# Performance work log

Measured on AMD Instinct MI355X. Metric: run time of the kernel, lower is better.

## Reference

```python
import jax, jax.numpy as jnp
import numpy as np


def setup_inputs() -> dict:
    key = jax.random.key(0)
    ks = jax.random.split(key, 9)
    H, A = 1024, 1024
    Ns, Ne, M = 8192, 4096, 8192
    s = 1.0 / np.sqrt(H)
    return {
        "attendee_stmts": jax.random.normal(ks[0], (Ns, H), jnp.float32),
        "attendee_eres": jax.random.normal(ks[1], (Ne, H), jnp.float32),
        "attender": jax.random.normal(ks[2], (M, H), jnp.float32),
        "W_ss": jax.random.normal(ks[3], (H, H), jnp.float32) * s,
        "b_ss": jnp.zeros((H,), jnp.float32),
        "W_es": jax.random.normal(ks[4], (H, H), jnp.float32) * s,
        "b_es": jnp.zeros((H,), jnp.float32),
        "W_lin": jax.random.normal(ks[5], (A, 3 * H), jnp.float32) * (1.0 / np.sqrt(3 * H)),
        "b_lin": jnp.zeros((A,), jnp.float32),
    }


def reference(attendee_stmts, attendee_eres, attender,
              W_ss, b_ss, W_es, b_es, W_lin, b_lin):
    # Bilinear scores: Linear(attendees) @ attender^T -> [N, M]
    scores_ss = (attendee_stmts @ W_ss.T + b_ss) @ attender.T   # [Ns, M]
    scores_es = (attendee_eres @ W_es.T + b_es) @ attender.T    # [Ne, M]
    # Softmax over attendee dim (dim 0), dropout p=0 -> identity
    w_ss = jax.nn.softmax(scores_ss, axis=0)
    w_es = jax.nn.softmax(scores_es, axis=0)
    # Context vectors: weights^T @ attendees -> [M, H]
    ctx_ss = w_ss.T @ attendee_stmts
    ctx_es = w_es.T @ attendee_eres
    # concat + Linear + tanh -> [M, A]
    cat = jnp.concatenate([attender, ctx_ss, ctx_es], axis=-1)  # [M, 3H]
    return jnp.tanh(cat @ W_lin.T + b_lin)
```

## Files before the change

kernel.cpp:

```cpp
#include <hip/hip_runtime.h>
#include <hip/hip_fp16.h>
#include <stdint.h>

typedef _Float16 f16;
typedef _Float16 f16x8 __attribute__((ext_vector_type(8)));
typedef _Float16 f16x4 __attribute__((ext_vector_type(4)));
typedef float f32x4 __attribute__((ext_vector_type(4)));
typedef short s16x8 __attribute__((ext_vector_type(8)));
typedef unsigned short u16x8 __attribute__((ext_vector_type(8)));
typedef unsigned short u16x4 __attribute__((ext_vector_type(4)));

#define DEV __device__ __forceinline__

DEV void gload_lds16(const void* g, void* l) {
    __builtin_amdgcn_global_load_lds(
        (const __attribute__((address_space(1))) void*)g,
        (__attribute__((address_space(3))) void*)l, 16, 0, 0);
}

DEV unsigned short f32_to_bf16(float x) {
    union { float f; unsigned int u; } c; c.f = x;
    unsigned int r = (c.u + 0x7FFFu + ((c.u >> 16) & 1u)) >> 16;
    return (unsigned short)r;
}
DEV float bf16_to_f32(unsigned short h) {
    union { unsigned int u; float f; } c; c.u = ((unsigned int)h) << 16;
    return c.f;
}

DEV void swz_map(int bid, int nx, int ny, int& bm, int& bn) {
    const int xcd = bid & 7;
    const int j = bid >> 3;
    const int py = ny >> 3;
    bm = xcd * py + j / nx;
    bn = j % nx;
}

__global__ __launch_bounds__(256, 2) void gemm_score(
    const float* __restrict__ A, const f16* __restrict__ Bhi,
    const f16* __restrict__ Blo, int ldc, unsigned short* __restrict__ Sp)
{
    __shared__ alignas(16) f16 As_hi[128 * 32];
    __shared__ alignas(16) f16 As_lo[128 * 32];
    __shared__ alignas(16) f16 Bs_hi[128 * 32];
    __shared__ alignas(16) f16 Bs_lo[128 * 32];
    const int t = threadIdx.x;
    const int lane = t & 63;
    const int w = t >> 6;
    const size_t m0 = (size_t)blockIdx.y * 128;
    const size_t n0 = (size_t)blockIdx.x * 128;
    const int wrow = (w >> 1) * 64;
    const int wcol = (w & 1) * 64;

    f32x4 acc[4][4] = {};

    for (int k0 = 0; k0 < 1024; k0 += 32) {
        __syncthreads();
#pragma unroll
        for (int p = 0; p < 4; ++p) {
            const int idx = p * 256 + t;
            const int row = idx >> 3;
            const int col4 = (idx & 7) << 2;
            const f32x4 v = *(const f32x4*)&A[(m0 + row) * 1024 + k0 + col4];
            f16x4 h, l;
#pragma unroll
            for (int j = 0; j < 4; ++j) {
                h[j] = (f16)v[j];
                l[j] = (f16)(v[j] - (float)h[j]);
            }
            *(f16x4*)&As_hi[idx * 4] = h;
            *(f16x4*)&As_lo[idx * 4] = l;
        }
#pragma unroll
        for (int i = 0; i < 2; ++i) {
            const int c = i * 256 + t;
            const int row = c >> 2;
            const int col = (c & 3) << 3;
            const int loff = (i * 256 + w * 64) * 8;
            const size_t gb = (n0 + row) * (size_t)1024 + k0 + col;
            gload_lds16(Bhi + gb, &Bs_hi[loff]);
            gload_lds16(Blo + gb, &Bs_lo[loff]);
        }
        __syncthreads();
        const int fr = lane & 15;
        const int fk = (lane >> 4) << 3;
        f16x8 ah[4], al[4], bh[4], bl[4];
#pragma unroll
        for (int x = 0; x < 4; ++x) {
            ah[x] = *(const f16x8*)&As_hi[(wrow + x * 16 + fr) * 32 + fk];
            al[x] = *(const f16x8*)&As_lo[(wrow + x * 16 + fr) * 32 + fk];
            bh[x] = *(const f16x8*)&Bs_hi[(wcol + x * 16 + fr) * 32 + fk];
            bl[x] = *(const f16x8*)&Bs_lo[(wcol + x * 16 + fr) * 32 + fk];
        }
#pragma unroll
        for (int mi = 0; mi < 4; ++mi)
#pragma unroll
            for (int ni = 0; ni < 4; ++ni) {
                acc[mi][ni] = __builtin_amdgcn_mfma_f32_16x16x32_f16(ah[mi], bh[ni], acc[mi][ni], 0, 0, 0);
                acc[mi][ni] = __builtin_amdgcn_mfma_f32_16x16x32_f16(al[mi], bh[ni], acc[mi][ni], 0, 0, 0);
                acc[mi][ni] = __builtin_amdgcn_mfma_f32_16x16x32_f16(ah[mi], bl[ni], acc[mi][ni], 0, 0, 0);
            }
    }

    const int fr = lane & 15;
    const int fq = lane >> 4;
#pragma unroll
    for (int mi = 0; mi < 4; ++mi)
#pragma unroll
        for (int ni = 0; ni < 4; ++ni)
#pragma unroll
            for (int r = 0; r < 4; ++r) {
                const size_t row = m0 + wrow + mi * 16 + fq * 4 + r;
                const size_t col = n0 + wcol + ni * 16 + fr;
                const float e = __expf(acc[mi][ni][r] - 150.f);
                Sp[row * (size_t)ldc + col] = f32_to_bf16(e);
            }
}

__global__ __launch_bounds__(256, 2) void gemm_proj(
    const float* __restrict__ A, const float* __restrict__ B,
    const float* __restrict__ bias, int ldc,
    f16* __restrict__ Phi, f16* __restrict__ Plo)
{
    __shared__ alignas(16) f16 As_hi[128 * 32];
    __shared__ alignas(16) f16 As_lo[128 * 32];
    __shared__ alignas(16) f16 Bs_hi[128 * 32];
    __shared__ alignas(16) f16 Bs_lo[128 * 32];
    const int t = threadIdx.x;
    const int lane = t & 63;
    const int w = t >> 6;
    const size_t m0 = (size_t)blockIdx.y * 128;
    const size_t n0 = (size_t)blockIdx.x * 128;
    const int wrow = (w >> 1) * 64;
    const int wcol = (w & 1) * 64;

    f32x4 acc[4][4] = {};

    for (int k0 = 0; k0 < 1024; k0 += 32) {
        __syncthreads();
#pragma unroll
        for (int p = 0; p < 4; ++p) {
            const int idx = p * 256 + t;
            const int row = idx >> 3;
            const int col4 = (idx & 7) << 2;
            const f32x4 va = *(const f32x4*)&A[(m0 + row) * 1024 + k0 + col4];
            const f32x4 vb = *(const f32x4*)&B[(n0 + row) * 1024 + k0 + col4];
            f16x4 ha, la, hb, lb;
#pragma unroll
            for (int j = 0; j < 4; ++j) {
                ha[j] = (f16)va[j];
                la[j] = (f16)(va[j] - (float)ha[j]);
                hb[j] = (f16)vb[j];
                lb[j] = (f16)(vb[j] - (float)hb[j]);
            }
            *(f16x4*)&As_hi[idx * 4] = ha;
            *(f16x4*)&As_lo[idx * 4] = la;
            *(f16x4*)&Bs_hi[idx * 4] = hb;
            *(f16x4*)&Bs_lo[idx * 4] = lb;
        }
        __syncthreads();
        const int fr = lane & 15;
        const int fk = (lane >> 4) << 3;
        f16x8 ah[4], al[4], bh[4], bl[4];
#pragma unroll
        for (int x = 0; x < 4; ++x) {
            ah[x] = *(const f16x8*)&As_hi[(wrow + x * 16 + fr) * 32 + fk];
            al[x] = *(const f16x8*)&As_lo[(wrow + x * 16 + fr) * 32 + fk];
            bh[x] = *(const f16x8*)&Bs_hi[(wcol + x * 16 + fr) * 32 + fk];
            bl[x] = *(const f16x8*)&Bs_lo[(wcol + x * 16 + fr) * 32 + fk];
        }
#pragma unroll
        for (int mi = 0; mi < 4; ++mi)
#pragma unroll
            for (int ni = 0; ni < 4; ++ni) {
                acc[mi][ni] = __builtin_amdgcn_mfma_f32_16x16x32_f16(ah[mi], bh[ni], acc[mi][ni], 0, 0, 0);
                acc[mi][ni] = __builtin_amdgcn_mfma_f32_16x16x32_f16(al[mi], bh[ni], acc[mi][ni], 0, 0, 0);
                acc[mi][ni] = __builtin_amdgcn_mfma_f32_16x16x32_f16(ah[mi], bl[ni], acc[mi][ni], 0, 0, 0);
            }
    }

    const int fr = lane & 15;
    const int fq = lane >> 4;
#pragma unroll
    for (int mi = 0; mi < 4; ++mi)
#pragma unroll
        for (int ni = 0; ni < 4; ++ni)
#pragma unroll
            for (int r = 0; r < 4; ++r) {
                const size_t row = m0 + wrow + mi * 16 + fq * 4 + r;
                const size_t col = n0 + wcol + ni * 16 + fr;
                float v = acc[mi][ni][r] + bias[col];
                const f16 h = (f16)v;
                Phi[row * (size_t)ldc + col] = h;
                Plo[row * (size_t)ldc + col] = (f16)(v - (float)h);
            }
}

__global__ __launch_bounds__(256, 4) void gemm_ctx_sk(
    const unsigned short* __restrict__ A, const unsigned short* __restrict__ B,
    const float* __restrict__ isum, int ldk, int K2,
    f16* __restrict__ P0, f16* __restrict__ P1)
{
    __shared__ alignas(16) unsigned short LA[2][128 * 32];
    __shared__ alignas(16) unsigned short LB[2][128 * 32];
    const int t = threadIdx.x;
    const int lane = t & 63;
    const int w = t >> 6;
    const int kh = blockIdx.x >> 9;
    int bm, bn;
    swz_map(blockIdx.x & 511, 8, 64, bm, bn);
    const size_t m0 = (size_t)bm * 128;
    const size_t n0 = (size_t)bn * 128;
    const size_t koff = (size_t)kh * K2;
    const int wrow = (w >> 1) * 64;
    const int wcol = (w & 1) * 64;
    const int fr = lane & 15;
    const int bslot = lane >> 4;
    f16* __restrict__ P = kh ? P1 : P0;

    const int s0 = t, s1 = 256 + t;
    const int r0 = s0 >> 2, c0 = s0 & 3;
    const int r1 = s1 >> 2, c1 = s1 & 3;
    const size_t ga0 = (m0 + r0) * (size_t)ldk + koff + ((c0 ^ (r0 & 3)) << 3);
    const size_t ga1 = (m0 + r1) * (size_t)ldk + koff + ((c1 ^ (r1 & 3)) << 3);
    const size_t gb0 = (n0 + r0) * (size_t)ldk + koff + ((c0 ^ (r0 & 3)) << 3);
    const size_t gb1 = (n0 + r1) * (size_t)ldk + koff + ((c1 ^ (r1 & 3)) << 3);

    f32x4 acc[4][4] = {};

    auto stage = [&](int kt, int b) {
        const int k0 = kt << 5;
        gload_lds16(A + ga0 + k0, &LA[b][(size_t)s0 * 8]);
        gload_lds16(A + ga1 + k0, &LA[b][(size_t)s1 * 8]);
        gload_lds16(B + gb0 + k0, &LB[b][(size_t)s0 * 8]);
        gload_lds16(B + gb1 + k0, &LB[b][(size_t)s1 * 8]);
    };

    auto compute = [&](int b) {
        s16x8 a[4], bb[4];
#pragma unroll
        for (int x = 0; x < 4; ++x) {
            const int ra = wrow + x * 16 + fr;
            const int rb = wcol + x * 16 + fr;
            a[x]  = *(const s16x8*)&LA[b][ra * 32 + ((bslot ^ (ra & 3)) << 3)];
            bb[x] = *(const s16x8*)&LB[b][rb * 32 + ((bslot ^ (rb & 3)) << 3)];
        }
#pragma unroll
        for (int mi = 0; mi < 4; ++mi)
#pragma unroll
            for (int ni = 0; ni < 4; ++ni)
                acc[mi][ni] = __builtin_amdgcn_mfma_f32_16x16x32_bf16(a[mi], bb[ni], acc[mi][ni], 0, 0, 0);
    };

    const int NT = K2 >> 5;
    stage(0, 0);
#pragma unroll 1
    for (int kt = 0; kt < NT; kt += 2) {
        __syncthreads();
        if (kt + 1 < NT) stage(kt + 1, 1);
        __builtin_amdgcn_s_setprio(1);
        compute(0);
        __builtin_amdgcn_s_setprio(0);
        __syncthreads();
        if (kt + 2 < NT) stage(kt + 2, 0);
        __builtin_amdgcn_s_setprio(1);
        compute(1);
        __builtin_amdgcn_s_setprio(0);
    }

    const int fq = lane >> 4;
#pragma unroll
    for (int mi = 0; mi < 4; ++mi)
#pragma unroll
        for (int ni = 0; ni < 4; ++ni)
#pragma unroll
            for (int r = 0; r < 4; ++r) {
                const size_t row = m0 + wrow + mi * 16 + fq * 4 + r;
                const size_t col = n0 + wcol + ni * 16 + fr;
                P[row * 1024 + col] = (f16)(acc[mi][ni][r] * isum[row]);
            }
}

__global__ __launch_bounds__(256, 2) void gemm_final_sk(
    const float* __restrict__ A0, const f16* __restrict__ A1,
    const f16* __restrict__ A2, const f16* __restrict__ B,
    f16* __restrict__ P0, f16* __restrict__ P1)
{
    __shared__ alignas(16) f16 As[128 * 32];
    __shared__ alignas(16) f16 Bs[128 * 32];
    const int t = threadIdx.x;
    const int lane = t & 63;
    const int w = t >> 6;
    const int kh = blockIdx.x >> 9;
    int bm, bn;
    swz_map(blockIdx.x & 511, 8, 64, bm, bn);
    const size_t m0 = (size_t)bm * 128;
    const size_t n0 = (size_t)bn * 128;
    const int wrow = (w >> 1) * 64;
    const int wcol = (w & 1) * 64;
    const int kBeg = kh * 1536;
    f16* __restrict__ P = kh ? P1 : P0;

    f32x4 acc[4][4] = {};

    for (int k0 = kBeg; k0 < kBeg + 1536; k0 += 32) {
        const int kl = k0 & 1023;
        __syncthreads();
        if (k0 < 1024) {
#pragma unroll
            for (int p = 0; p < 4; ++p) {
                const int idx = p * 256 + t;
                const int row = idx >> 3;
                const int col4 = (idx & 7) << 2;
                const f32x4 v = *(const f32x4*)&A0[(m0 + row) * 1024 + kl + col4];
                f16x4 h;
#pragma unroll
                for (int j = 0; j < 4; ++j) h[j] = (f16)v[j];
                *(f16x4*)&As[idx * 4] = h;
            }
        } else {
            const f16* Aseg = (k0 < 2048) ? A1 : A2;
#pragma unroll
            for (int i = 0; i < 2; ++i) {
                const int c = i * 256 + t;
                const int row = c >> 2;
                const int col = (c & 3) << 3;
                const int loff = (i * 256 + w * 64) * 8;
                gload_lds16(Aseg + (m0 + row) * (size_t)1024 + kl + col, &As[loff]);
            }
        }
#pragma unroll
        for (int i = 0; i < 2; ++i) {
            const int c = i * 256 + t;
            const int row = c >> 2;
            const int col = (c & 3) << 3;
            const int loff = (i * 256 + w * 64) * 8;
            gload_lds16(B + (n0 + row) * (size_t)3072 + k0 + col, &Bs[loff]);
        }
        __syncthreads();
        const int fr = lane & 15;
        const int fk = (lane >> 4) << 3;
        f16x8 a[4], b[4];
#pragma unroll
        for (int x = 0; x < 4; ++x) {
            a[x] = *(const f16x8*)&As[(wrow + x * 16 + fr) * 32 + fk];
            b[x] = *(const f16x8*)&Bs[(wcol + x * 16 + fr) * 32 + fk];
        }
#pragma unroll
        for (int mi = 0; mi < 4; ++mi)
#pragma unroll
            for (int ni = 0; ni < 4; ++ni)
                acc[mi][ni] = __builtin_amdgcn_mfma_f32_16x16x32_f16(a[mi], b[ni], acc[mi][ni], 0, 0, 0);
    }

    const int fr = lane & 15;
    const int fq = lane >> 4;
#pragma unroll
    for (int mi = 0; mi < 4; ++mi)
#pragma unroll
        for (int ni = 0; ni < 4; ++ni)
#pragma unroll
            for (int r = 0; r < 4; ++r) {
                const size_t row = m0 + wrow + mi * 16 + fq * 4 + r;
                const size_t col = n0 + wcol + ni * 16 + fr;
                P[row * 1024 + col] = (f16)acc[mi][ni][r];
            }
}

__global__ __launch_bounds__(256) void reduce_add_f16(
    const f16* __restrict__ p0, const f16* __restrict__ p1,
    f16* __restrict__ out, int n8)
{
    for (int i = blockIdx.x * 256 + threadIdx.x; i < n8; i += gridDim.x * 256) {
        const f16x8 a = *(const f16x8*)&p0[(size_t)i * 8];
        const f16x8 b = *(const f16x8*)&p1[(size_t)i * 8];
        f16x8 o;
#pragma unroll
        for (int j = 0; j < 8; ++j) o[j] = (f16)((float)a[j] + (float)b[j]);
        *(f16x8*)&out[(size_t)i * 8] = o;
    }
}

__global__ __launch_bounds__(256) void reduce_tanh_f32(
    const f16* __restrict__ p0, const f16* __restrict__ p1,
    const float* __restrict__ bias, float* __restrict__ out, int n4)
{
    for (int i = blockIdx.x * 256 + threadIdx.x; i < n4; i += gridDim.x * 256) {
        const size_t e = (size_t)i * 4;
        const f16x4 a = *(const f16x4*)&p0[e];
        const f16x4 b = *(const f16x4*)&p1[e];
        f32x4 o;
#pragma unroll
        for (int j = 0; j < 4; ++j)
            o[j] = tanhf((float)a[j] + (float)b[j] + bias[(e + j) & 1023]);
        *(f32x4*)&out[e] = o;
    }
}

template <int C>
__global__ __launch_bounds__(256) void rowsum_inv(
    const unsigned short* __restrict__ E, float* __restrict__ inv)
{
    const unsigned short* e = E + (size_t)blockIdx.x * (C * 2048);
    const int t = threadIdx.x;
    float sm = 0.f;
#pragma unroll
    for (int i = 0; i < C; ++i) {
        const u16x8 v = *(const u16x8*)&e[(t + i * 256) * 8];
#pragma unroll
        for (int j = 0; j < 8; ++j) sm += bf16_to_f32(v[j]);
    }
#pragma unroll
    for (int off = 32; off; off >>= 1) sm += __shfl_xor(sm, off);
    __shared__ float red[4];
    if ((t & 63) == 0) red[t >> 6] = sm;
    __syncthreads();
    if (t == 0) {
        const float s = (red[0] + red[1]) + (red[2] + red[3]);
        inv[blockIdx.x] = 1.f / s;
    }
}

__global__ __launch_bounds__(256) void transpose_f32_to_bf16(
    const float* __restrict__ X, unsigned short* __restrict__ Xt, int N, int H)
{
    __shared__ float tile[64][65];
    const int n0 = blockIdx.x * 64;
    const int h0 = blockIdx.y * 64;
    const int tx = threadIdx.x & 15;
    const int ty = threadIdx.x >> 4;
#pragma unroll
    for (int i = 0; i < 4; ++i) {
        const int r = ty + i * 16;
        const f32x4 vv = *(const f32x4*)&X[(size_t)(n0 + r) * H + h0 + tx * 4];
        tile[r][tx * 4 + 0] = vv[0];
        tile[r][tx * 4 + 1] = vv[1];
        tile[r][tx * 4 + 2] = vv[2];
        tile[r][tx * 4 + 3] = vv[3];
    }
    __syncthreads();
#pragma unroll
    for (int i = 0; i < 4; ++i) {
        const int hh = ty + i * 16;
        u16x4 o;
        o[0] = f32_to_bf16(tile[tx * 4 + 0][hh]);
        o[1] = f32_to_bf16(tile[tx * 4 + 1][hh]);
        o[2] = f32_to_bf16(tile[tx * 4 + 2][hh]);
        o[3] = f32_to_bf16(tile[tx * 4 + 3][hh]);
        *(u16x4*)&Xt[(size_t)(h0 + hh) * N + n0 + tx * 4] = o;
    }
}

__global__ __launch_bounds__(256) void conv_f32_f16(
    const float* __restrict__ X, f16* __restrict__ Y)
{
    const size_t i = ((size_t)blockIdx.x * 256 + threadIdx.x) * 4;
    const f32x4 v = *(const f32x4*)&X[i];
    f16x4 h;
#pragma unroll
    for (int j = 0; j < 4; ++j) h[j] = (f16)v[j];
    *(f16x4*)&Y[i] = h;
}

extern "C" void kernel_launch(void* const* d_in, const int* in_sizes, int n_in,
                              void* d_out, int out_size, void* d_ws, size_t ws_size,
                              hipStream_t stream)
{
    (void)in_sizes; (void)n_in; (void)out_size;
    constexpr int Ns = 8192, Ne = 4096, M = 8192, H = 1024, K3 = 3072, AO = 1024;

    const float* Xss  = (const float*)d_in[0];
    const float* Xes  = (const float*)d_in[1];
    const float* Att  = (const float*)d_in[2];
    const float* Wss  = (const float*)d_in[3];
    const float* bss  = (const float*)d_in[4];
    const float* Wes  = (const float*)d_in[5];
    const float* bes  = (const float*)d_in[6];
    const float* Wlin = (const float*)d_in[7];
    const float* blin = (const float*)d_in[8];
    float* Out = (float*)d_out;

    char* base = (char*)d_ws;
    size_t off = 0;
    auto carve = [&](size_t bytes) {
        char* r = base + off;
        off = (off + bytes + 255) & ~(size_t)255;
        return r;
    };

    f16* Wl16            = (f16*)carve((size_t)AO * K3 * 2);
    unsigned short* Vtss = (unsigned short*)carve((size_t)H * Ns * 2);
    unsigned short* Vtes = (unsigned short*)carve((size_t)H * Ne * 2);
    f16* Pes_hi          = (f16*)carve((size_t)Ne * H * 2);
    f16* Pes_lo          = (f16*)carve((size_t)Ne * H * 2);
    char* PssRg          = carve((size_t)2 * Ns * H * 2);
    char* E              = carve((size_t)M * Ns * 2);
    f16* Ctxss           = (f16*)carve((size_t)M * H * 2);
    f16* Ctxes           = (f16*)carve((size_t)M * H * 2);
    float* isum_ss       = (float*)carve((size_t)M * 4);
    float* isum_es       = (float*)carve((size_t)M * 4);
    if (off > ws_size) return;

    f16* Pss_hi = (f16*)PssRg;
    f16* Pss_lo = Pss_hi + (size_t)Ns * H;
    f16* ctxP0  = (f16*)PssRg;
    f16* ctxP1  = ctxP0 + (size_t)M * H;
    unsigned short* Sss = (unsigned short*)E;
    unsigned short* Ses = (unsigned short*)E;
    f16* fnP0   = (f16*)E;
    f16* fnP1   = fnP0 + (size_t)M * AO;

    const int n8 = (M * H) / 8;
    const int n4 = (M * AO) / 4;

    conv_f32_f16<<<(AO * K3) / 1024, 256, 0, stream>>>(Wlin, Wl16);
    transpose_f32_to_bf16<<<dim3(Ns / 64, H / 64), 256, 0, stream>>>(Xss, Vtss, Ns, H);
    transpose_f32_to_bf16<<<dim3(Ne / 64, H / 64), 256, 0, stream>>>(Xes, Vtes, Ne, H);

    gemm_proj<<<dim3(H / 128, Ns / 128), 256, 0, stream>>>(Xss, Wss, bss, H, Pss_hi, Pss_lo);
    gemm_proj<<<dim3(H / 128, Ne / 128), 256, 0, stream>>>(Xes, Wes, bes, H, Pes_hi, Pes_lo);

    gemm_score<<<dim3(Ns / 128, M / 128), 256, 0, stream>>>(Att, Pss_hi, Pss_lo, Ns, Sss);
    rowsum_inv<4><<<M, 256, 0, stream>>>(Sss, isum_ss);
    gemm_ctx_sk<<<1024, 256, 0, stream>>>(Sss, Vtss, isum_ss, Ns, Ns / 2, ctxP0, ctxP1);
    reduce_add_f16<<<1024, 256, 0, stream>>>(ctxP0, ctxP1, Ctxss, n8);

    gemm_score<<<dim3(Ne / 128, M / 128), 256, 0, stream>>>(Att, Pes_hi, Pes_lo, Ne, Ses);
    rowsum_inv<2><<<M, 256, 0, stream>>>(Ses, isum_es);
    gemm_ctx_sk<<<1024, 256, 0, stream>>>(Ses, Vtes, isum_es, Ne, Ne / 2, ctxP0, ctxP1);
    reduce_add_f16<<<1024, 256, 0, stream>>>(ctxP0, ctxP1, Ctxes, n8);

    gemm_final_sk<<<1024, 256, 0, stream>>>(Att, Ctxss, Ctxes, Wl16, fnP0, fnP1);
    reduce_tanh_f32<<<1024, 256, 0, stream>>>(fnP0, fnP1, blin, Out, n4);
}
```

Baseline: 1.067 ms.

## Fuse softmax row sums into score GEMM epilogue and pre-split attender to f16

```diff
diff --git a/kernel.cpp b/kernel.cpp
--- a/kernel.cpp
+++ b/kernel.cpp
@@ -23,10 +23,6 @@
     unsigned int r = (c.u + 0x7FFFu + ((c.u >> 16) & 1u)) >> 16;
     return (unsigned short)r;
 }
-DEV float bf16_to_f32(unsigned short h) {
-    union { unsigned int u; float f; } c; c.u = ((unsigned int)h) << 16;
-    return c.f;
-}
 
 DEV void swz_map(int bid, int nx, int ny, int& bm, int& bn) {
     const int xcd = bid & 7;
@@ -36,9 +32,36 @@
     bn = j % nx;
 }
 
-__global__ __launch_bounds__(256, 2) void gemm_score(
+DEV void score_epilogue(f32x4 (&acc)[4][4], size_t m0, size_t n0,
+                        int wrow, int wcol, int lane, int ldc,
+                        unsigned short* __restrict__ Sp,
+                        float* __restrict__ rsum)
+{
+    const int fr = lane & 15;
+    const int fq = lane >> 4;
+#pragma unroll
+    for (int mi = 0; mi < 4; ++mi)
+#pragma unroll
+        for (int r = 0; r < 4; ++r) {
+            const size_t row = m0 + wrow + mi * 16 + fq * 4 + r;
+            float rowacc = 0.f;
+#pragma unroll
+            for (int ni = 0; ni < 4; ++ni) {
+                const size_t col = n0 + wcol + ni * 16 + fr;
+                const float e = __expf(acc[mi][ni][r] - 150.f);
+                Sp[row * (size_t)ldc + col] = f32_to_bf16(e);
+                rowacc += e;
+            }
+#pragma unroll
+            for (int m = 1; m < 16; m <<= 1) rowacc += __shfl_xor(rowacc, m);
+            if (fr == 0) atomicAdd(&rsum[row], rowacc);
+        }
+}
+
+__global__ __launch_bounds__(256, 2) void gemm_score_rs(
     const float* __restrict__ A, const f16* __restrict__ Bhi,
-    const f16* __restrict__ Blo, int ldc, unsigned short* __restrict__ Sp)
+    const f16* __restrict__ Blo, int ldc, unsigned short* __restrict__ Sp,
+    float* __restrict__ rsum)
 {
     __shared__ alignas(16) f16 As_hi[128 * 32];
     __shared__ alignas(16) f16 As_lo[128 * 32];
@@ -102,19 +125,65 @@
             }
     }
 
-    const int fr = lane & 15;
-    const int fq = lane >> 4;
-#pragma unroll
-    for (int mi = 0; mi < 4; ++mi)
-#pragma unroll
-        for (int ni = 0; ni < 4; ++ni)
-#pragma unroll
-            for (int r = 0; r < 4; ++r) {
-                const size_t row = m0 + wrow + mi * 16 + fq * 4 + r;
-                const size_t col = n0 + wcol + ni * 16 + fr;
-                const float e = __expf(acc[mi][ni][r] - 150.f);
-                Sp[row * (size_t)ldc + col] = f32_to_bf16(e);
-            }
+    score_epilogue(acc, m0, n0, wrow, wcol, lane, ldc, Sp, rsum);
+}
+
+__global__ __launch_bounds__(256, 2) void gemm_score_4op(
+    const f16* __restrict__ Ahi, const f16* __restrict__ Alo,
+    const f16* __restrict__ Bhi, const f16* __restrict__ Blo,
+    int ldc, unsigned short* __restrict__ Sp, float* __restrict__ rsum)
+{
+    __shared__ alignas(16) f16 As_hi[128 * 32];
+    __shared__ alignas(16) f16 As_lo[128 * 32];
+    __shared__ alignas(16) f16 Bs_hi[128 * 32];
+    __shared__ alignas(16) f16 Bs_lo[128 * 32];
+    const int t = threadIdx.x;
+    const int lane = t & 63;
+    const int w = t >> 6;
+    const size_t m0 = (size_t)blockIdx.y * 128;
+    const size_t n0 = (size_t)blockIdx.x * 128;
+    const int wrow = (w >> 1) * 64;
+    const int wcol = (w & 1) * 64;
+
+    f32x4 acc[4][4] = {};
+
+    for (int k0 = 0; k0 < 1024; k0 += 32) {
+        __syncthreads();
+#pragma unroll
+        for (int i = 0; i < 2; ++i) {
+            const int c = i * 256 + t;
+            const int row = c >> 2;
+            const int col = (c & 3) << 3;
+            const int loff = (i * 256 + w * 64) * 8;
+            const size_t ga = (m0 + row) * (size_t)1024 + k0 + col;
+            const size_t gb = (n0 + row) * (size_t)1024 + k0 + col;
+            gload_lds16(Ahi + ga, &As_hi[loff]);
+            gload_lds16(Alo + ga, &As_lo[loff]);
+            gload_lds16(Bhi + gb, &Bs_hi[loff]);
+            gload_lds16(Blo + gb, &Bs_lo[loff]);
+        }
+        __syncthreads();
+        const int fr = lane & 15;
+        const int fk = (lane >> 4) << 3;
+        f16x8 ah[4], al[4], bh[4], bl[4];
+#pragma unroll
+        for (int x = 0; x < 4; ++x) {
+            ah[x] = *(const f16x8*)&As_hi[(wrow + x * 16 + fr) * 32 + fk];
+            al[x] = *(const f16x8*)&As_lo[(wrow + x * 16 + fr) * 32 + fk];
+            bh[x] = *(const f16x8*)&Bs_hi[(wcol + x * 16 + fr) * 32 + fk];
+            bl[x] = *(const f16x8*)&Bs_lo[(wcol + x * 16 + fr) * 32 + fk];
+        }
+#pragma unroll
+        for (int mi = 0; mi < 4; ++mi)
+#pragma unroll
+            for (int ni = 0; ni < 4; ++ni) {
+                acc[mi][ni] = __builtin_amdgcn_mfma_f32_16x16x32_f16(ah[mi], bh[ni], acc[mi][ni], 0, 0, 0);
+                acc[mi][ni] = __builtin_amdgcn_mfma_f32_16x16x32_f16(al[mi], bh[ni], acc[mi][ni], 0, 0, 0);
+                acc[mi][ni] = __builtin_amdgcn_mfma_f32_16x16x32_f16(ah[mi], bl[ni], acc[mi][ni], 0, 0, 0);
+            }
+    }
+
+    score_epilogue(acc, m0, n0, wrow, wcol, lane, ldc, Sp, rsum);
 }
 
 __global__ __launch_bounds__(256, 2) void gemm_proj(
@@ -397,28 +466,29 @@
     }
 }
 
-template <int C>
-__global__ __launch_bounds__(256) void rowsum_inv(
-    const unsigned short* __restrict__ E, float* __restrict__ inv)
-{
-    const unsigned short* e = E + (size_t)blockIdx.x * (C * 2048);
-    const int t = threadIdx.x;
-    float sm = 0.f;
-#pragma unroll
-    for (int i = 0; i < C; ++i) {
-        const u16x8 v = *(const u16x8*)&e[(t + i * 256) * 8];
-#pragma unroll
-        for (int j = 0; j < 8; ++j) sm += bf16_to_f32(v[j]);
-    }
-#pragma unroll
-    for (int off = 32; off; off >>= 1) sm += __shfl_xor(sm, off);
-    __shared__ float red[4];
-    if ((t & 63) == 0) red[t >> 6] = sm;
-    __syncthreads();
-    if (t == 0) {
-        const float s = (red[0] + red[1]) + (red[2] + red[3]);
-        inv[blockIdx.x] = 1.f / s;
-    }
+__global__ __launch_bounds__(256) void zero_f32(float* __restrict__ p, int n) {
+    const int i = blockIdx.x * 256 + threadIdx.x;
+    if (i < n) p[i] = 0.f;
+}
+
+__global__ __launch_bounds__(256) void inv_f32(float* __restrict__ p, int n) {
+    const int i = blockIdx.x * 256 + threadIdx.x;
+    if (i < n) p[i] = 1.f / p[i];
+}
+
+__global__ __launch_bounds__(256) void split_f32_f16(
+    const float* __restrict__ X, f16* __restrict__ hi, f16* __restrict__ lo)
+{
+    const size_t i = ((size_t)blockIdx.x * 256 + threadIdx.x) * 4;
+    const f32x4 v = *(const f32x4*)&X[i];
+    f16x4 h, l;
+#pragma unroll
+    for (int j = 0; j < 4; ++j) {
+        h[j] = (f16)v[j];
+        l[j] = (f16)(v[j] - (float)h[j]);
+    }
+    *(f16x4*)&hi[i] = h;
+    *(f16x4*)&lo[i] = l;
 }
 
 __global__ __launch_bounds__(256) void transpose_f32_to_bf16(
@@ -491,24 +561,30 @@
     f16* Wl16            = (f16*)carve((size_t)AO * K3 * 2);
     unsigned short* Vtss = (unsigned short*)carve((size_t)H * Ns * 2);
     unsigned short* Vtes = (unsigned short*)carve((size_t)H * Ne * 2);
-    f16* Pes_hi          = (f16*)carve((size_t)Ne * H * 2);
-    f16* Pes_lo          = (f16*)carve((size_t)Ne * H * 2);
+    char* PesRg          = carve((size_t)2 * Ne * H * 2);
     char* PssRg          = carve((size_t)2 * Ns * H * 2);
     char* E              = carve((size_t)M * Ns * 2);
-    f16* Ctxss           = (f16*)carve((size_t)M * H * 2);
+    char* CtxssRg        = carve((size_t)M * H * 2);
     f16* Ctxes           = (f16*)carve((size_t)M * H * 2);
-    float* isum_ss       = (float*)carve((size_t)M * 4);
-    float* isum_es       = (float*)carve((size_t)M * 4);
+    float* sum_ss        = (float*)carve((size_t)M * 4);
+    float* sum_es        = (float*)carve((size_t)M * 4);
     if (off > ws_size) return;
 
+    f16* Pes_hi = (f16*)PesRg;
+    f16* Pes_lo = Pes_hi + (size_t)Ne * H;
+    f16* Att_hi = (f16*)PesRg;
+    f16* Att_lo = (f16*)CtxssRg;
     f16* Pss_hi = (f16*)PssRg;
     f16* Pss_lo = Pss_hi + (size_t)Ns * H;
-    f16* ctxP0  = (f16*)PssRg;
-    f16* ctxP1  = ctxP0 + (size_t)M * H;
+    unsigned short* Ses = (unsigned short*)E;
     unsigned short* Sss = (unsigned short*)E;
-    unsigned short* Ses = (unsigned short*)E;
-    f16* fnP0   = (f16*)E;
-    f16* fnP1   = fnP0 + (size_t)M * AO;
+    f16* esP0  = (f16*)(E + (size_t)M * Ne * 2);
+    f16* esP1  = esP0 + (size_t)M * H;
+    f16* ssP0  = (f16*)PssRg;
+    f16* ssP1  = ssP0 + (size_t)M * H;
+    f16* Ctxss = (f16*)CtxssRg;
+    f16* fnP0  = (f16*)E;
+    f16* fnP1  = fnP0 + (size_t)M * AO;
 
     const int n8 = (M * H) / 8;
     const int n4 = (M * AO) / 4;
@@ -516,19 +592,24 @@
     conv_f32_f16<<<(AO * K3) / 1024, 256, 0, stream>>>(Wlin, Wl16);
     transpose_f32_to_bf16<<<dim3(Ns / 64, H / 64), 256, 0, stream>>>(Xss, Vtss, Ns, H);
     transpose_f32_to_bf16<<<dim3(Ne / 64, H / 64), 256, 0, stream>>>(Xes, Vtes, Ne, H);
+    zero_f32<<<(2 * M) / 256, 256, 0, stream>>>(sum_ss, 2 * M);
 
     gemm_proj<<<dim3(H / 128, Ns / 128), 256, 0, stream>>>(Xss, Wss, bss, H, Pss_hi, Pss_lo);
     gemm_proj<<<dim3(H / 128, Ne / 128), 256, 0, stream>>>(Xes, Wes, bes, H, Pes_hi, Pes_lo);
 
-    gemm_score<<<dim3(Ns / 128, M / 128), 256, 0, stream>>>(Att, Pss_hi, Pss_lo, Ns, Sss);
-    rowsum_inv<4><<<M, 256, 0, stream>>>(Sss, isum_ss);
-    gemm_ctx_sk<<<1024, 256, 0, stream>>>(Sss, Vtss, isum_ss, Ns, Ns / 2, ctxP0, ctxP1);
-    reduce_add_f16<<<1024, 256, 0, stream>>>(ctxP0, ctxP1, Ctxss, n8);
-
-    gemm_score<<<dim3(Ne / 128, M / 128), 256, 0, stream>>>(Att, Pes_hi, Pes_lo, Ne, Ses);
-    rowsum_inv<2><<<M, 256, 0, stream>>>(Ses, isum_es);
-    gemm_ctx_sk<<<1024, 256, 0, stream>>>(Ses, Vtes, isum_es, Ne, Ne / 2, ctxP0, ctxP1);
-    reduce_add_f16<<<1024, 256, 0, stream>>>(ctxP0, ctxP1, Ctxes, n8);
+    gemm_score_rs<<<dim3(Ne / 128, M / 128), 256, 0, stream>>>(
+        Att, Pes_hi, Pes_lo, Ne, Ses, sum_es);
+    inv_f32<<<M / 256, 256, 0, stream>>>(sum_es, M);
+    gemm_ctx_sk<<<1024, 256, 0, stream>>>(Ses, Vtes, sum_es, Ne, Ne / 2, esP0, esP1);
+    reduce_add_f16<<<1024, 256, 0, stream>>>(esP0, esP1, Ctxes, n8);
+
+    split_f32_f16<<<(M * H) / 1024, 256, 0, stream>>>(Att, Att_hi, Att_lo);
+
+    gemm_score_4op<<<dim3(Ns / 128, M / 128), 256, 0, stream>>>(
+        Att_hi, Att_lo, Pss_hi, Pss_lo, Ns, Sss, sum_ss);
+    inv_f32<<<M / 256, 256, 0, stream>>>(sum_ss, M);
+    gemm_ctx_sk<<<1024, 256, 0, stream>>>(Sss, Vtss, sum_ss, Ns, Ns / 2, ssP0, ssP1);
+    reduce_add_f16<<<1024, 256, 0, stream>>>(ssP0, ssP1, Ctxss, n8);
 
     gemm_final_sk<<<1024, 256, 0, stream>>>(Att, Ctxss, Ctxes, Wl16, fnP0, fnP1);
     reduce_tanh_f32<<<1024, 256, 0, stream>>>(fnP0, fnP1, blin, Out, n4);
```

Measured after the change: 1.075 ms. Within noise of the previous version (+0.8%).
